# Kernel tuning notes

Measured on AMD Instinct MI355X. Metric: run time of the kernel, lower is better.

The kernel has to match this reference:

```python
import jax, jax.numpy as jnp
import numpy as np

DIM = 1024
SEQ_LEN = 2048
NUM_HEAD = 16
HEAD_DIM = 64
B = 4


def setup_inputs() -> dict:
    key = jax.random.key(0)
    ks = jax.random.split(key, 9)
    hd = NUM_HEAD * HEAD_DIM
    s_in = 1.0 / np.sqrt(DIM)
    s_o = 1.0 / np.sqrt(hd)
    return {
        "x": jax.random.normal(ks[0], (B, SEQ_LEN, DIM), dtype=jnp.float32),
        "q_w": jax.random.uniform(ks[1], (hd, DIM), jnp.float32, -s_in, s_in),
        "q_b": jax.random.uniform(ks[2], (hd,), jnp.float32, -s_in, s_in),
        "k_w": jax.random.uniform(ks[3], (hd, DIM), jnp.float32, -s_in, s_in),
        "k_b": jax.random.uniform(ks[4], (hd,), jnp.float32, -s_in, s_in),
        "v_w": jax.random.uniform(ks[5], (hd, DIM), jnp.float32, -s_in, s_in),
        "v_b": jax.random.uniform(ks[6], (hd,), jnp.float32, -s_in, s_in),
        "o_w": jax.random.uniform(ks[7], (DIM, hd), jnp.float32, -s_o, s_o),
        "o_b": jax.random.uniform(ks[8], (DIM,), jnp.float32, -s_o, s_o),
    }


def reference(x, q_w, q_b, k_w, k_b, v_w, v_b, o_w, o_b):
    Bn, T, C = x.shape
    # QKV projections (torch Linear: x @ W^T + b)
    q = (x @ q_w.T + q_b).reshape(Bn, T, NUM_HEAD, HEAD_DIM).transpose(0, 2, 1, 3)
    k = (x @ k_w.T + k_b).reshape(Bn, T, NUM_HEAD, HEAD_DIM).transpose(0, 2, 1, 3)
    v = (x @ v_w.T + v_b).reshape(Bn, T, NUM_HEAD, HEAD_DIM).transpose(0, 2, 1, 3)
    scale = HEAD_DIM ** -0.5
    attn = jnp.einsum("bhqd,bhkd->bhqk", q, k) * scale  # (B,H,T,T)
    causal = jnp.tril(jnp.ones((T, T), dtype=bool))
    attn = jnp.where(causal[None, None, :, :], attn, -jnp.inf)
    p = jax.nn.softmax(attn, axis=-1)  # stable softmax (max-subtracted)
    out = jnp.einsum("bhqk,bhkd->bhqd", p, v)
    out = out.transpose(0, 2, 1, 3).reshape(Bn, T, NUM_HEAD * HEAD_DIM)
    return out @ o_w.T + o_b
```

## Files before the change

### kernel.cpp

```cpp
#include <hip/hip_runtime.h>
#include <stdint.h>

typedef short short8 __attribute__((ext_vector_type(8)));
typedef float f32x4 __attribute__((ext_vector_type(4)));

__device__ __forceinline__ unsigned short f2bf(float f) {
    unsigned int u = __float_as_uint(f);
    u += 0x7fffu + ((u >> 16) & 1u);
    return (unsigned short)(u >> 16);
}

__device__ __forceinline__ void gld_lds16(const unsigned short* g, unsigned short* l) {
    __builtin_amdgcn_global_load_lds((const __attribute__((address_space(1))) unsigned int*)g,
                                     (__attribute__((address_space(3))) unsigned int*)l,
                                     16, 0, 0);
}

#define QSCL 0.18033688011112042f

__global__ __launch_bounds__(256) void cvt_all(const float* __restrict__ x,
                                               const float* __restrict__ qw, const float* __restrict__ kw,
                                               const float* __restrict__ vw, const float* __restrict__ ow,
                                               const float* __restrict__ qb, const float* __restrict__ kb,
                                               const float* __restrict__ vb,
                                               unsigned short* __restrict__ Xb,
                                               unsigned short* __restrict__ Wqkv,
                                               unsigned short* __restrict__ Owb,
                                               float* __restrict__ bqkv) {
    int i = blockIdx.x * 256 + threadIdx.x;
    const float* src; uint2* dst; int j;
    if (i < 2097152)      { src = x;  dst = (uint2*)Xb;                j = i; }
    else if (i < 2359296) { src = qw; dst = (uint2*)Wqkv;              j = i - 2097152; }
    else if (i < 2621440) { src = kw; dst = (uint2*)(Wqkv + 1048576);  j = i - 2359296; }
    else if (i < 2883584) { src = vw; dst = (uint2*)(Wqkv + 2097152);  j = i - 2621440; }
    else if (i < 3145728) { src = ow; dst = (uint2*)Owb;               j = i - 2883584; }
    else {
        int t = i - 3145728;
        const float4* bs = (t < 256) ? (const float4*)qb : (t < 512) ? (const float4*)kb : (const float4*)vb;
        ((float4*)bqkv)[t] = bs[t & 255];
        return;
    }
    float4 v = ((const float4*)src)[j];
    unsigned int lo = (unsigned int)f2bf(v.x) | ((unsigned int)f2bf(v.y) << 16);
    unsigned int hi = (unsigned int)f2bf(v.z) | ((unsigned int)f2bf(v.w) << 16);
    dst[j] = make_uint2(lo, hi);
}

template<int MODE>
__global__ __launch_bounds__(256) void gemm_bt(const unsigned short* __restrict__ A,
                                               const unsigned short* __restrict__ Bm,
                                               const float* __restrict__ bias,
                                               void* __restrict__ C0,
                                               unsigned short* __restrict__ VtOut,
                                               int M, int N, int K)
{
    __shared__ __align__(16) unsigned short As[128 * 64];
    __shared__ __align__(16) unsigned short Bs[128 * 64];
    const int tid  = threadIdx.x;
    const int bm   = blockIdx.x, bn = blockIdx.y;
    const int lane = tid & 63, w = tid >> 6;
    const int wm   = w >> 1, wn = w & 1;
    const int quad = lane >> 4, l15 = lane & 15;

    f32x4 acc[4][4];
#pragma unroll
    for (int mt = 0; mt < 4; mt++)
#pragma unroll
        for (int nt = 0; nt < 4; nt++)
            acc[mt][nt] = (f32x4){0.f, 0.f, 0.f, 0.f};

    const int kTiles = K >> 6;
    for (int kt = 0; kt < kTiles; ++kt) {
        __syncthreads();
#pragma unroll
        for (int i = 0; i < 4; i++) {
            int G  = i * 256 + tid;
            int m  = G >> 3, g = G & 7;
            int gs = g ^ (m & 7);
            int Gb = i * 256 + (w << 6);
            gld_lds16(A  + (size_t)(bm * 128 + m) * K + kt * 64 + gs * 8, &As[Gb * 8]);
            gld_lds16(Bm + (size_t)(bn * 128 + m) * K + kt * 64 + gs * 8, &Bs[Gb * 8]);
        }
        __syncthreads();
#pragma unroll
        for (int ks = 0; ks < 2; ++ks) {
            short8 af[4], bfr[4];
#pragma unroll
            for (int mt = 0; mt < 4; mt++) {
                int m = wm * 64 + mt * 16 + l15;
                af[mt] = *(const short8*)&As[m * 64 + (((ks * 4 + quad) ^ (l15 & 7)) << 3)];
            }
#pragma unroll
            for (int nt = 0; nt < 4; nt++) {
                int n = wn * 64 + nt * 16 + l15;
                bfr[nt] = *(const short8*)&Bs[n * 64 + (((ks * 4 + quad) ^ (l15 & 7)) << 3)];
            }
#pragma unroll
            for (int mt = 0; mt < 4; mt++)
#pragma unroll
                for (int nt = 0; nt < 4; nt++)
                    acc[mt][nt] = __builtin_amdgcn_mfma_f32_16x16x32_bf16(af[mt], bfr[nt], acc[mt][nt], 0, 0, 0);
        }
    }
    const int row0 = bm * 128 + wm * 64, col0 = bn * 128 + wn * 64;
#pragma unroll
    for (int nt = 0; nt < 4; nt++) {
        int col = col0 + nt * 16 + l15;
        float bv = bias[col];
#pragma unroll
        for (int mt = 0; mt < 4; mt++) {
            if (MODE == 1 && col >= 2048) {
                int row = row0 + mt * 16 + quad * 4;
                int b = row >> 11, t = row & 2047;
                ushort4 pk;
                pk.x = f2bf(acc[mt][nt][0] + bv);
                pk.y = f2bf(acc[mt][nt][1] + bv);
                pk.z = f2bf(acc[mt][nt][2] + bv);
                pk.w = f2bf(acc[mt][nt][3] + bv);
                *(ushort4*)(VtOut + (size_t)(b * 1024 + (col - 2048)) * 2048 + t) = pk;
            } else {
#pragma unroll
                for (int r = 0; r < 4; r++) {
                    int row = row0 + mt * 16 + quad * 4 + r;
                    float v = acc[mt][nt][r] + bv;
                    if (MODE == 1) {
                        if (col < 1024) v *= QSCL;
                        ((unsigned short*)C0)[(size_t)row * 2048 + col] = f2bf(v);
                    } else {
                        ((float*)C0)[(size_t)row * N + col] = v;
                    }
                }
            }
        }
    }
}

#define NEG_RAW (-1e30f)
__global__ __launch_bounds__(256) void attn_mfma(const unsigned short* __restrict__ QK,
                                                 const unsigned short* __restrict__ Vt,
                                                 unsigned short* __restrict__ O)
{
    __shared__ __align__(16) unsigned short Kb[2][64 * 64];
    __shared__ __align__(16) unsigned short Vb[2][64 * 64];
    __shared__ __align__(16) unsigned short Ps[4 * 32 * 72];
    const int tid  = threadIdx.x;
    const int lane = tid & 63, w = tid >> 6;
    const int quad = lane >> 4, l15 = lane & 15;
    const int bh   = blockIdx.x;
    const int b    = bh >> 4, h = bh & 15;
    const int qt   = (int)gridDim.y - 1 - (int)blockIdx.y;
    const int qbase = qt * 128 + w * 32;

    const unsigned short* Qp = QK + (size_t)(b * 2048) * 2048 + h * 64;
    const unsigned short* Kp = Qp + 1024;
    const unsigned short* Vp = Vt + (size_t)(bh * 64) * 2048;
    unsigned short* Pw = Ps + w * 32 * 72;

    short8 qf[2][2];
#pragma unroll
    for (int mt = 0; mt < 2; mt++)
#pragma unroll
        for (int kk = 0; kk < 2; kk++)
            qf[mt][kk] = *(const short8*)(Qp + (size_t)(qbase + mt * 16 + l15) * 2048 + kk * 32 + quad * 8);

    short8 ones;
#pragma unroll
    for (int j = 0; j < 8; j++) ones[j] = (short)0x3F80;

    f32x4 oacc[2][4], lacc[2];
#pragma unroll
    for (int mt = 0; mt < 2; mt++) {
        lacc[mt] = (f32x4){0.f, 0.f, 0.f, 0.f};
#pragma unroll
        for (int nt = 0; nt < 4; nt++) oacc[mt][nt] = (f32x4){0.f, 0.f, 0.f, 0.f};
    }

    const int ktend   = 2 * qt + 1;
    const int ktmax_w = (qbase + 31) >> 6;

#pragma unroll
    for (int i = 0; i < 2; i++) {
        int G = i * 256 + tid;
        int r = G >> 3, g = G & 7, gs = g ^ (r & 7);
        int Gb = i * 256 + (w << 6);
        gld_lds16(Kp + (size_t)r * 2048 + gs * 8, &Kb[0][Gb * 8]);
        gld_lds16(Vp + (size_t)r * 2048 + gs * 8, &Vb[0][Gb * 8]);
    }
    __syncthreads();

    for (int kt = 0; kt <= ktend; ++kt) {
        const int cur = kt & 1;
        if (kt < ktend) {
            const unsigned short* Kn = Kp + (size_t)((kt + 1) * 64) * 2048;
            const unsigned short* Vn = Vp + (kt + 1) * 64;
#pragma unroll
            for (int i = 0; i < 2; i++) {
                int G = i * 256 + tid;
                int r = G >> 3, g = G & 7, gs = g ^ (r & 7);
                int Gb = i * 256 + (w << 6);
                gld_lds16(Kn + (size_t)r * 2048 + gs * 8, &Kb[cur ^ 1][Gb * 8]);
                gld_lds16(Vn + (size_t)r * 2048 + gs * 8, &Vb[cur ^ 1][Gb * 8]);
            }
        }
        if (kt <= ktmax_w) {
            const unsigned short* Kc = Kb[cur];
            const unsigned short* Vc = Vb[cur];
            const int kbase = kt * 64;
            const bool diag = (kbase + 63 > qbase);
#pragma unroll
            for (int nt = 0; nt < 4; nt++) {
                short8 kf0, kf1;
                {
                    int key = nt * 16 + l15, sw = key & 7;
                    kf0 = *(const short8*)&Kc[key * 64 + ((quad ^ sw) << 3)];
                    kf1 = *(const short8*)&Kc[key * 64 + (((4 + quad) ^ sw) << 3)];
                }
#pragma unroll
                for (int mt = 0; mt < 2; mt++) {
                    if (diag && kbase + nt * 16 > qbase + mt * 16 + 15) {
                        *(uint2*)&Pw[(mt * 16 + l15) * 72 + nt * 16 + quad * 4] = make_uint2(0u, 0u);
                        continue;
                    }
                    f32x4 sacc = (f32x4){0.f, 0.f, 0.f, 0.f};
                    sacc = __builtin_amdgcn_mfma_f32_16x16x32_bf16(kf0, qf[mt][0], sacc, 0, 0, 0);
                    sacc = __builtin_amdgcn_mfma_f32_16x16x32_bf16(kf1, qf[mt][1], sacc, 0, 0, 0);
                    if (diag) {
                        const int qg = qbase + mt * 16 + l15;
#pragma unroll
                        for (int r = 0; r < 4; r++)
                            if (kbase + nt * 16 + quad * 4 + r > qg) sacc[r] = NEG_RAW;
                    }
                    float p0 = __builtin_exp2f(sacc[0]);
                    float p1 = __builtin_exp2f(sacc[1]);
                    float p2 = __builtin_exp2f(sacc[2]);
                    float p3 = __builtin_exp2f(sacc[3]);
                    unsigned int lo = __builtin_amdgcn_perm(__float_as_uint(p1), __float_as_uint(p0), 0x07060302u);
                    unsigned int hi = __builtin_amdgcn_perm(__float_as_uint(p3), __float_as_uint(p2), 0x07060302u);
                    *(uint2*)&Pw[(mt * 16 + l15) * 72 + nt * 16 + quad * 4] = make_uint2(lo, hi);
                }
            }
#pragma unroll
            for (int kv = 0; kv < 2; kv++) {
                short8 pf0 = *(const short8*)&Pw[l15 * 72 + kv * 32 + quad * 8];
                short8 pf1 = *(const short8*)&Pw[(16 + l15) * 72 + kv * 32 + quad * 8];
                lacc[0] = __builtin_amdgcn_mfma_f32_16x16x32_bf16(ones, pf0, lacc[0], 0, 0, 0);
                lacc[1] = __builtin_amdgcn_mfma_f32_16x16x32_bf16(ones, pf1, lacc[1], 0, 0, 0);
#pragma unroll
                for (int nt = 0; nt < 4; nt++) {
                    int d = nt * 16 + l15;
                    short8 vf = *(const short8*)&Vc[d * 64 + (((kv * 4 + quad) ^ (d & 7)) << 3)];
                    oacc[0][nt] = __builtin_amdgcn_mfma_f32_16x16x32_bf16(vf, pf0, oacc[0][nt], 0, 0, 0);
                    oacc[1][nt] = __builtin_amdgcn_mfma_f32_16x16x32_bf16(vf, pf1, oacc[1][nt], 0, 0, 0);
                }
            }
        }
        __syncthreads();
    }

#pragma unroll
    for (int mt = 0; mt < 2; mt++) {
        const float inv = 1.f / lacc[mt][0];
        unsigned short* op = O + (size_t)(b * 2048 + qbase + mt * 16 + l15) * 1024 + h * 64;
#pragma unroll
        for (int nt = 0; nt < 4; nt++) {
            ushort4 pk;
            pk.x = f2bf(oacc[mt][nt][0] * inv);
            pk.y = f2bf(oacc[mt][nt][1] * inv);
            pk.z = f2bf(oacc[mt][nt][2] * inv);
            pk.w = f2bf(oacc[mt][nt][3] * inv);
            *(ushort4*)(op + nt * 16 + quad * 4) = pk;
        }
    }
}

extern "C" void kernel_launch(void* const* d_in, const int* in_sizes, int n_in,
                              void* d_out, int out_size, void* d_ws, size_t ws_size,
                              hipStream_t stream)
{
    const float* x   = (const float*)d_in[0];
    const float* q_w = (const float*)d_in[1];
    const float* q_b = (const float*)d_in[2];
    const float* k_w = (const float*)d_in[3];
    const float* k_b = (const float*)d_in[4];
    const float* v_w = (const float*)d_in[5];
    const float* v_b = (const float*)d_in[6];
    const float* o_w = (const float*)d_in[7];
    const float* o_b = (const float*)d_in[8];
    float* out = (float*)d_out;

    unsigned short* Xb   = (unsigned short*)d_ws;
    unsigned short* Wqkv = Xb + 8388608;
    unsigned short* Owb  = Wqkv + 3145728;
    float*          bqkv = (float*)(Owb + 1048576);
    unsigned short* QK   = (unsigned short*)(bqkv + 3072);
    unsigned short* Vtg  = QK + 16777216;
    unsigned short* Abf  = Vtg + 8388608;

    cvt_all<<<12291, 256, 0, stream>>>(x, q_w, k_w, v_w, o_w, q_b, k_b, v_b,
                                       Xb, Wqkv, Owb, bqkv);
    gemm_bt<1><<<dim3(64, 24), 256, 0, stream>>>(Xb, Wqkv, bqkv, QK, Vtg, 8192, 3072, 1024);
    attn_mfma<<<dim3(64, 16), 256, 0, stream>>>(QK, Vtg, Abf);
    gemm_bt<0><<<dim3(64, 8), 256, 0, stream>>>(Abf, Owb, o_b, out, nullptr, 8192, 1024, 1024);
}
```

Measured before the change: 269.4 us.

## Switch attention to 32x32 MFMA with register-resident P via permlane32 swap

Rewrites the attention inner loop to use 32x32x16 bf16 MFMA tiles instead of 16x16x32. The P tile is repacked in registers with permlane32_swap rather than going through LDS, and row sums are accumulated in VALU instead of a ones-matrix MFMA. It also adds wave priority hints around the compute section and a launch_bounds occupancy hint. This is meant to remove LDS round-trips and redundant MFMAs, at the cost of higher register pressure from the 16-wide accumulators.

```diff
diff --git a/kernel.cpp b/kernel.cpp
--- a/kernel.cpp
+++ b/kernel.cpp
@@ -3,6 +3,9 @@
 
 typedef short short8 __attribute__((ext_vector_type(8)));
 typedef float f32x4 __attribute__((ext_vector_type(4)));
+typedef float f32x16 __attribute__((ext_vector_type(16)));
+typedef unsigned int uint2v __attribute__((ext_vector_type(2)));
+typedef unsigned int uint4v __attribute__((ext_vector_type(4)));
 
 __device__ __forceinline__ unsigned short f2bf(float f) {
     unsigned int u = __float_as_uint(f);
@@ -136,16 +139,16 @@
 }
 
 #define NEG_RAW (-1e30f)
-__global__ __launch_bounds__(256) void attn_mfma(const unsigned short* __restrict__ QK,
-                                                 const unsigned short* __restrict__ Vt,
-                                                 unsigned short* __restrict__ O)
+__global__ __launch_bounds__(256, 4) void attn_mfma(const unsigned short* __restrict__ QK,
+                                                    const unsigned short* __restrict__ Vt,
+                                                    unsigned short* __restrict__ O)
 {
     __shared__ __align__(16) unsigned short Kb[2][64 * 64];
     __shared__ __align__(16) unsigned short Vb[2][64 * 64];
-    __shared__ __align__(16) unsigned short Ps[4 * 32 * 72];
     const int tid  = threadIdx.x;
     const int lane = tid & 63, w = tid >> 6;
-    const int quad = lane >> 4, l15 = lane & 15;
+    const int hi   = lane >> 5, l31 = lane & 31;
+    const int s7   = lane & 7;
     const int bh   = blockIdx.x;
     const int b    = bh >> 4, h = bh & 15;
     const int qt   = (int)gridDim.y - 1 - (int)blockIdx.y;
@@ -154,26 +157,21 @@
     const unsigned short* Qp = QK + (size_t)(b * 2048) * 2048 + h * 64;
     const unsigned short* Kp = Qp + 1024;
     const unsigned short* Vp = Vt + (size_t)(bh * 64) * 2048;
-    unsigned short* Pw = Ps + w * 32 * 72;
-
-    short8 qf[2][2];
-#pragma unroll
-    for (int mt = 0; mt < 2; mt++)
-#pragma unroll
-        for (int kk = 0; kk < 2; kk++)
-            qf[mt][kk] = *(const short8*)(Qp + (size_t)(qbase + mt * 16 + l15) * 2048 + kk * 32 + quad * 8);
-
-    short8 ones;
-#pragma unroll
-    for (int j = 0; j < 8; j++) ones[j] = (short)0x3F80;
-
-    f32x4 oacc[2][4], lacc[2];
-#pragma unroll
-    for (int mt = 0; mt < 2; mt++) {
-        lacc[mt] = (f32x4){0.f, 0.f, 0.f, 0.f};
-#pragma unroll
-        for (int nt = 0; nt < 4; nt++) oacc[mt][nt] = (f32x4){0.f, 0.f, 0.f, 0.f};
-    }
+
+    short8 qf[4];
+    {
+        const unsigned short* qrow = Qp + (size_t)(qbase + l31) * 2048 + hi * 8;
+#pragma unroll
+        for (int dk = 0; dk < 4; dk++)
+            qf[dk] = *(const short8*)(qrow + dk * 16);
+    }
+
+    f32x16 oacc[2];
+#pragma unroll
+    for (int i = 0; i < 2; i++)
+#pragma unroll
+        for (int r = 0; r < 16; r++) oacc[i][r] = 0.f;
+    float lsum = 0.f;
 
     const int ktend   = 2 * qt + 1;
     const int ktmax_w = (qbase + 31) >> 6;
@@ -203,72 +201,81 @@
             }
         }
         if (kt <= ktmax_w) {
+            __builtin_amdgcn_s_setprio(1);
             const unsigned short* Kc = Kb[cur];
             const unsigned short* Vc = Vb[cur];
             const int kbase = kt * 64;
-            const bool diag = (kbase + 63 > qbase);
-#pragma unroll
-            for (int nt = 0; nt < 4; nt++) {
-                short8 kf0, kf1;
+#pragma unroll
+            for (int sub = 0; sub < 2; sub++) {
+                const int kb0 = kbase + sub * 32;
+                if (kb0 > qbase + 31) continue;
+                f32x16 sacc;
+#pragma unroll
+                for (int r = 0; r < 16; r++) sacc[r] = 0.f;
+                const unsigned short* kr = &Kc[(sub * 32 + l31) * 64];
+#pragma unroll
+                for (int dk = 0; dk < 4; dk++) {
+                    short8 kf = *(const short8*)(kr + (((dk * 2 + hi) ^ s7) << 3));
+                    sacc = __builtin_amdgcn_mfma_f32_32x32x16_bf16(kf, qf[dk], sacc, 0, 0, 0);
+                }
+                if (kb0 + 31 > qbase) {
+                    const int qg = qbase + l31;
+                    const int kb = kb0 + 4 * hi;
+#pragma unroll
+                    for (int r = 0; r < 16; r++) {
+                        int key = kb + (r & 3) + 8 * (r >> 2);
+                        if (key > qg) sacc[r] = NEG_RAW;
+                    }
+                }
+#pragma unroll
+                for (int r = 0; r < 16; r++) sacc[r] = __builtin_exp2f(sacc[r]);
                 {
-                    int key = nt * 16 + l15, sw = key & 7;
-                    kf0 = *(const short8*)&Kc[key * 64 + ((quad ^ sw) << 3)];
-                    kf1 = *(const short8*)&Kc[key * 64 + (((4 + quad) ^ sw) << 3)];
-                }
-#pragma unroll
-                for (int mt = 0; mt < 2; mt++) {
-                    if (diag && kbase + nt * 16 > qbase + mt * 16 + 15) {
-                        *(uint2*)&Pw[(mt * 16 + l15) * 72 + nt * 16 + quad * 4] = make_uint2(0u, 0u);
-                        continue;
+                    float s0 = (sacc[0] + sacc[1]) + (sacc[2] + sacc[3]);
+                    float s1 = (sacc[4] + sacc[5]) + (sacc[6] + sacc[7]);
+                    float s2 = (sacc[8] + sacc[9]) + (sacc[10] + sacc[11]);
+                    float s3 = (sacc[12] + sacc[13]) + (sacc[14] + sacc[15]);
+                    lsum += (s0 + s1) + (s2 + s3);
+                }
+                unsigned int pk[8];
+#pragma unroll
+                for (int t2 = 0; t2 < 8; t2++)
+                    pk[t2] = __builtin_amdgcn_perm(__float_as_uint(sacc[2 * t2 + 1]),
+                                                   __float_as_uint(sacc[2 * t2]), 0x07060302u);
+                uint2v r0 = __builtin_amdgcn_permlane32_swap(pk[0], pk[2], false, false);
+                uint2v r1 = __builtin_amdgcn_permlane32_swap(pk[1], pk[3], false, false);
+                uint2v r2 = __builtin_amdgcn_permlane32_swap(pk[4], pk[6], false, false);
+                uint2v r3 = __builtin_amdgcn_permlane32_swap(pk[5], pk[7], false, false);
+                short8 pf[2];
+                { uint4v u; u.x = r0.x; u.y = r1.x; u.z = r0.y; u.w = r1.y; pf[0] = __builtin_bit_cast(short8, u); }
+                { uint4v u; u.x = r2.x; u.y = r3.x; u.z = r2.y; u.w = r3.y; pf[1] = __builtin_bit_cast(short8, u); }
+#pragma unroll
+                for (int kv = 0; kv < 2; kv++) {
+#pragma unroll
+                    for (int dsub = 0; dsub < 2; dsub++) {
+                        const int d = dsub * 32 + l31;
+                        short8 vf = *(const short8*)&Vc[d * 64 + (((sub * 4 + kv * 2 + hi) ^ s7) << 3)];
+                        oacc[dsub] = __builtin_amdgcn_mfma_f32_32x32x16_bf16(vf, pf[kv], oacc[dsub], 0, 0, 0);
                     }
-                    f32x4 sacc = (f32x4){0.f, 0.f, 0.f, 0.f};
-                    sacc = __builtin_amdgcn_mfma_f32_16x16x32_bf16(kf0, qf[mt][0], sacc, 0, 0, 0);
-                    sacc = __builtin_amdgcn_mfma_f32_16x16x32_bf16(kf1, qf[mt][1], sacc, 0, 0, 0);
-                    if (diag) {
-                        const int qg = qbase + mt * 16 + l15;
-#pragma unroll
-                        for (int r = 0; r < 4; r++)
-                            if (kbase + nt * 16 + quad * 4 + r > qg) sacc[r] = NEG_RAW;
-                    }
-                    float p0 = __builtin_exp2f(sacc[0]);
-                    float p1 = __builtin_exp2f(sacc[1]);
-                    float p2 = __builtin_exp2f(sacc[2]);
-                    float p3 = __builtin_exp2f(sacc[3]);
-                    unsigned int lo = __builtin_amdgcn_perm(__float_as_uint(p1), __float_as_uint(p0), 0x07060302u);
-                    unsigned int hi = __builtin_amdgcn_perm(__float_as_uint(p3), __float_as_uint(p2), 0x07060302u);
-                    *(uint2*)&Pw[(mt * 16 + l15) * 72 + nt * 16 + quad * 4] = make_uint2(lo, hi);
-                }
-            }
-#pragma unroll
-            for (int kv = 0; kv < 2; kv++) {
-                short8 pf0 = *(const short8*)&Pw[l15 * 72 + kv * 32 + quad * 8];
-                short8 pf1 = *(const short8*)&Pw[(16 + l15) * 72 + kv * 32 + quad * 8];
-                lacc[0] = __builtin_amdgcn_mfma_f32_16x16x32_bf16(ones, pf0, lacc[0], 0, 0, 0);
-                lacc[1] = __builtin_amdgcn_mfma_f32_16x16x32_bf16(ones, pf1, lacc[1], 0, 0, 0);
-#pragma unroll
-                for (int nt = 0; nt < 4; nt++) {
-                    int d = nt * 16 + l15;
-                    short8 vf = *(const short8*)&Vc[d * 64 + (((kv * 4 + quad) ^ (d & 7)) << 3)];
-                    oacc[0][nt] = __builtin_amdgcn_mfma_f32_16x16x32_bf16(vf, pf0, oacc[0][nt], 0, 0, 0);
-                    oacc[1][nt] = __builtin_amdgcn_mfma_f32_16x16x32_bf16(vf, pf1, oacc[1][nt], 0, 0, 0);
-                }
-            }
+                }
+            }
+            __builtin_amdgcn_s_setprio(0);
         }
         __syncthreads();
     }
 
-#pragma unroll
-    for (int mt = 0; mt < 2; mt++) {
-        const float inv = 1.f / lacc[mt][0];
-        unsigned short* op = O + (size_t)(b * 2048 + qbase + mt * 16 + l15) * 1024 + h * 64;
-#pragma unroll
-        for (int nt = 0; nt < 4; nt++) {
-            ushort4 pk;
-            pk.x = f2bf(oacc[mt][nt][0] * inv);
-            pk.y = f2bf(oacc[mt][nt][1] * inv);
-            pk.z = f2bf(oacc[mt][nt][2] * inv);
-            pk.w = f2bf(oacc[mt][nt][3] * inv);
-            *(ushort4*)(op + nt * 16 + quad * 4) = pk;
+    uint2v lt = __builtin_amdgcn_permlane32_swap(__float_as_uint(lsum), __float_as_uint(lsum), false, false);
+    const float inv = 1.f / (__uint_as_float(lt.x) + __uint_as_float(lt.y));
+    unsigned short* op = O + (size_t)(b * 2048 + qbase + l31) * 1024 + h * 64;
+#pragma unroll
+    for (int dsub = 0; dsub < 2; dsub++) {
+#pragma unroll
+        for (int q4 = 0; q4 < 4; q4++) {
+            ushort4 pkv;
+            pkv.x = f2bf(oacc[dsub][q4 * 4 + 0] * inv);
+            pkv.y = f2bf(oacc[dsub][q4 * 4 + 1] * inv);
+            pkv.z = f2bf(oacc[dsub][q4 * 4 + 2] * inv);
+            pkv.w = f2bf(oacc[dsub][q4 * 4 + 3] * inv);
+            *(ushort4*)(op + dsub * 32 + q4 * 8 + hi * 4) = pkv;
         }
     }
 }
```

New measurement: 255.6 us. 1.05x faster.
